# Performance work log

Measured on AMD Instinct MI355X. Metric: run time of the kernel, lower is better.

Reference implementation:

```python
import jax, jax.numpy as jnp
import numpy as np

B, N, F, T, K, O = 8, 1024, 64, 32, 3, 64


def setup_inputs() -> dict:
    key = jax.random.key(0)
    k0, k1, k2, k3 = jax.random.split(key, 4)
    x = jax.random.normal(k0, (B, N, F, T), dtype=jnp.float32)
    spatial_attention = jax.random.uniform(k1, (B, N, N), dtype=jnp.float32)
    cheb = jax.random.normal(k2, (K, N, N), dtype=jnp.float32) * 0.1  # stacked T_k
    Theta = jax.random.normal(k3, (K, F, O), dtype=jnp.float32) * (1.0 / np.sqrt(F))
    return {"x": x, "spatial_attention": spatial_attention, "cheb": cheb, "Theta": Theta}


def reference(x, spatial_attention, cheb, Theta):
    # Original per-timestep, per-k loop computes:
    #   rhs[b,i,f] = sum_j (T_k[j,i] * att[b,j,i])... note: T_k_with_at.permute(0,2,1) @ x
    #   i.e. rhs[b,i,f,t] = sum_j T_k[j,i]*att[b,j,i]*x[b,j,f,t]
    # Vectorized over all timesteps t and Chebyshev orders k at once.
    rhs = jnp.einsum('kji,bji,bjft->bkift', cheb, spatial_attention, x)  # (B,K,N,F,T)
    out = jnp.einsum('bkift,kfo->biot', rhs, Theta)                      # sum over k,f
    return jax.nn.relu(out)  # (B,N,O,T)
```

## Files before the change

kernel.cpp:

```cpp
#include <hip/hip_runtime.h>
#include <stdint.h>

#define Bn 8
#define Nn 1024
#define Fn 64
#define Tn 32
#define Kn 3
#define On 64
#define Rn (Kn * Nn)
#define Cn (On * Tn)
#define NT (Rn / 32)

typedef __bf16 bf16x8 __attribute__((ext_vector_type(8)));
typedef float f32x4 __attribute__((ext_vector_type(4)));
typedef __attribute__((address_space(1))) void gvoid;
typedef __attribute__((address_space(3))) void lvoid;

union BF8 { bf16x8 v; ushort s[8]; uint4 q; };

static __device__ __forceinline__ ushort f2bf(float f) {
  uint32_t u = __float_as_uint(f);
  return (ushort)((u + 0x7FFFu + ((u >> 16) & 1u)) >> 16);
}

static __device__ __forceinline__ void glds(const ushort* g, ushort* l) {
  __builtin_amdgcn_global_load_lds((gvoid*)g, (lvoid*)l, 16, 0, 0);
}

__global__ void k_thetaT(const float* __restrict__ Theta, ushort* __restrict__ ThT) {
  int idx = blockIdx.x * 256 + threadIdx.x;
  if (idx < Kn * On * Fn) {
    int k = idx / (On * Fn);
    int rem = idx % (On * Fn);
    int o = rem / Fn, f = rem % Fn;
    ThT[idx] = f2bf(Theta[(k * Fn + f) * On + o]);
  }
}

__global__ __launch_bounds__(256) void k_prepW(const float* __restrict__ att,
                                               const float* __restrict__ cheb,
                                               ushort* __restrict__ Wt) {
  __shared__ float tile[32][33];
  int i0 = blockIdx.x * 32, j0 = blockIdx.y * 32, b = blockIdx.z;
  int tid = threadIdx.x;
  int ci = tid & 31, rj = tid >> 5;
  float av[4];
#pragma unroll
  for (int p = 0; p < 4; p++) {
    int j = j0 + rj + p * 8;
    av[p] = att[((size_t)b * Nn + j) * Nn + i0 + ci];
  }
  for (int k = 0; k < Kn; k++) {
#pragma unroll
    for (int p = 0; p < 4; p++) {
      int j = j0 + rj + p * 8;
      tile[rj + p * 8][ci] = av[p] * cheb[((size_t)k * Nn + j) * Nn + i0 + ci];
    }
    __syncthreads();
#pragma unroll
    for (int p = 0; p < 4; p++) {
      int i = i0 + rj + p * 8;
      Wt[((size_t)b * Nn + i) * Rn + (size_t)k * Nn + j0 + ci] = f2bf(tile[ci][rj + p * 8]);
    }
    __syncthreads();
  }
}

__global__ __launch_bounds__(512) void k_prepY(const float* __restrict__ x,
                                               const ushort* __restrict__ ThT,
                                               ushort* __restrict__ Yt) {
  __shared__ ushort ylds[1024 * 32];
  int jt = blockIdx.x, b = blockIdx.y;
  int j0 = jt * 32;
  int tid = threadIdx.x;
  int lane = tid & 63, w = tid >> 6;
  int l15 = lane & 15, l4 = lane >> 4;

  BF8 bfr[4][2][2];
#pragma unroll
  for (int jj = 0; jj < 4; jj++) {
    const float* xp = x + ((size_t)b * Nn + (j0 + w * 4 + jj)) * (Fn * Tn);
#pragma unroll
    for (int ks = 0; ks < 2; ks++)
#pragma unroll
      for (int tf = 0; tf < 2; tf++) {
        int t = tf * 16 + l15;
        int fb = ks * 32 + l4 * 8;
#pragma unroll
        for (int e = 0; e < 8; e++)
          bfr[jj][ks][tf].s[e] = f2bf(xp[(fb + e) * Tn + t]);
      }
  }

  for (int k = 0; k < Kn; k++) {
    for (int h = 0; h < 2; h++) {
      BF8 afr[2][2];
#pragma unroll
      for (int o2 = 0; o2 < 2; o2++)
#pragma unroll
        for (int ks = 0; ks < 2; ks++) {
          int o = h * 32 + o2 * 16 + l15;
          afr[o2][ks].q = *(const uint4*)&ThT[((size_t)k * On + o) * Fn + ks * 32 + l4 * 8];
        }
#pragma unroll
      for (int jj = 0; jj < 4; jj++) {
        f32x4 acc[2][2] = {};
#pragma unroll
        for (int ks = 0; ks < 2; ks++)
#pragma unroll
          for (int o2 = 0; o2 < 2; o2++)
#pragma unroll
            for (int tf = 0; tf < 2; tf++)
              acc[o2][tf] = __builtin_amdgcn_mfma_f32_16x16x32_bf16(
                  afr[o2][ks].v, bfr[jj][ks][tf].v, acc[o2][tf], 0, 0, 0);
#pragma unroll
        for (int o2 = 0; o2 < 2; o2++)
#pragma unroll
          for (int tf = 0; tf < 2; tf++)
#pragma unroll
            for (int q = 0; q < 4; q++) {
              int cl = (o2 * 16 + l4 * 4 + q) * Tn + tf * 16 + l15;
              ylds[cl * 32 + w * 4 + jj] = f2bf(acc[o2][tf][q]);
            }
      }
      __syncthreads();
      const uint32_t* yl32 = (const uint32_t*)ylds;
      uint32_t* Yt32 = (uint32_t*)Yt;
      int e = tid & 15, rowst = tid >> 4;
      for (int pass = 0; pass < 32; pass++) {
        int cl = pass * 32 + rowst;
        size_t off = ((size_t)b * Cn + (size_t)(h * 1024 + cl)) * Rn + (size_t)k * Nn + j0;
        Yt32[off / 2 + e] = yl32[cl * 16 + e];
      }
      __syncthreads();
    }
  }
}

__global__ __launch_bounds__(512, 2) void k_gemm(const ushort* __restrict__ Wt,
                                                 const ushort* __restrict__ Yt,
                                                 float* __restrict__ out) {
  extern __shared__ __align__(16) ushort smem[];
  ushort* As = smem;
  ushort* Bs = smem + 32768;

  int g = blockIdx.x;
  int b = g & 7, slot = g >> 3;
  int i0 = (slot & 3) * 256, c0 = (slot >> 2) * 256;
  int tid = threadIdx.x, lane = tid & 63, w = tid >> 6;
  int l15 = lane & 15, l4 = lane >> 4;
  int wm = w >> 2, wn = w & 3;

  const ushort* Ab = Wt + ((size_t)b * Nn + i0) * Rn;
  const ushort* Bb = Yt + ((size_t)b * Cn + c0) * Rn;

  int srow = tid >> 2, sch = (tid & 3) * 8;
  const ushort* aS = Ab + (size_t)srow * Rn + sch;
  const ushort* bS = Bb + (size_t)srow * Rn + sch;
  int dst0 = w * 512;

  int abase = (wm * 128 + l15) * 32 + l4 * 8;
  int bbase = (wn * 64 + l15) * 32 + l4 * 8;

  f32x4 acc[8][4] = {};

#define STAGE_A(t) { int bo_ = ((t) & 3) * 8192; \
    glds(aS + (size_t)(t) * 32, As + bo_ + dst0); \
    glds(aS + 128 * (size_t)Rn + (size_t)(t) * 32, As + bo_ + 4096 + dst0); }
#define STAGE_B(t) { int bo_ = ((t) & 3) * 8192; \
    glds(bS + (size_t)(t) * 32, Bs + bo_ + dst0); \
    glds(bS + 128 * (size_t)Rn + (size_t)(t) * 32, Bs + bo_ + 4096 + dst0); }

  STAGE_A(0); STAGE_B(0);
  STAGE_A(1); STAGE_B(1);
  STAGE_A(2); STAGE_B(2);
  asm volatile("s_waitcnt vmcnt(8)" ::: "memory");
  __builtin_amdgcn_s_barrier();

#define WINDOW(t, DOSTAGE) { \
    int bo_ = ((t) & 3) * 8192; \
    const ushort* Abuf = As + bo_; \
    const ushort* Bbuf = Bs + bo_; \
    BF8 bf[4], af[8]; \
    _Pragma("unroll") for (int n = 0; n < 4; n++) \
      bf[n].q = *(const uint4*)&Bbuf[bbase + n * 512]; \
    _Pragma("unroll") for (int m = 0; m < 4; m++) \
      af[m].q = *(const uint4*)&Abuf[abase + m * 512]; \
    if (DOSTAGE) STAGE_A((t) + 3); \
    __builtin_amdgcn_s_setprio(1); \
    _Pragma("unroll") for (int m = 0; m < 4; m++) \
      _Pragma("unroll") for (int n = 0; n < 4; n++) \
        acc[m][n] = __builtin_amdgcn_mfma_f32_16x16x32_bf16(af[m].v, bf[n].v, acc[m][n], 0, 0, 0); \
    __builtin_amdgcn_s_setprio(0); \
    _Pragma("unroll") for (int m = 4; m < 8; m++) \
      af[m].q = *(const uint4*)&Abuf[abase + m * 512]; \
    if (DOSTAGE) STAGE_B((t) + 3); \
    __builtin_amdgcn_s_setprio(1); \
    _Pragma("unroll") for (int m = 4; m < 8; m++) \
      _Pragma("unroll") for (int n = 0; n < 4; n++) \
        acc[m][n] = __builtin_amdgcn_mfma_f32_16x16x32_bf16(af[m].v, bf[n].v, acc[m][n], 0, 0, 0); \
    __builtin_amdgcn_s_setprio(0); \
  }

  for (int t = 0; t < NT - 3; ++t) {
    WINDOW(t, 1);
    asm volatile("s_waitcnt vmcnt(8)" ::: "memory");
    __builtin_amdgcn_s_barrier();
  }
  WINDOW(NT - 3, 0);
  asm volatile("s_waitcnt vmcnt(4)" ::: "memory");
  __builtin_amdgcn_s_barrier();
  WINDOW(NT - 2, 0);
  asm volatile("s_waitcnt vmcnt(0)" ::: "memory");
  __builtin_amdgcn_s_barrier();
  WINDOW(NT - 1, 0);

#undef WINDOW
#undef STAGE_A
#undef STAGE_B

  float* ob = out + (size_t)b * Nn * Cn;
#pragma unroll
  for (int m = 0; m < 8; m++) {
    int i = i0 + wm * 128 + m * 16 + l4 * 4;
#pragma unroll
    for (int n = 0; n < 4; n++) {
      int c = c0 + wn * 64 + n * 16 + l15;
#pragma unroll
      for (int q = 0; q < 4; q++)
        ob[(size_t)(i + q) * Cn + c] = fmaxf(acc[m][n][q], 0.0f);
    }
  }
}

extern "C" void kernel_launch(void* const* d_in, const int* in_sizes, int n_in,
                              void* d_out, int out_size, void* d_ws, size_t ws_size,
                              hipStream_t stream) {
  const float* x     = (const float*)d_in[0];
  const float* att   = (const float*)d_in[1];
  const float* cheb  = (const float*)d_in[2];
  const float* Theta = (const float*)d_in[3];
  float* out = (float*)d_out;

  char* ws = (char*)d_ws;
  ushort* ThT = (ushort*)ws;
  ushort* Wt  = (ushort*)(ws + 65536);
  ushort* Yt  = (ushort*)(ws + 65536 + 50331648ull);

  hipFuncSetAttribute((const void*)k_gemm, hipFuncAttributeMaxDynamicSharedMemorySize, 131072);

  k_thetaT<<<48, 256, 0, stream>>>(Theta, ThT);
  k_prepW<<<dim3(32, 32, 8), 256, 0, stream>>>(att, cheb, Wt);
  k_prepY<<<dim3(32, 8), 512, 0, stream>>>(x, ThT, Yt);
  k_gemm<<<256, 512, 131072, stream>>>(Wt, Yt, out);
}
```

Baseline: 169.9 us.

## Restructure GEMM pipeline to K=64 double-buffered swizzled tiles and reuse cheb across batches

The main GEMM moves from 32-wide K steps with a 4-deep LDS ring to 64-wide K steps with double buffering and an XOR-swizzled LDS layout. Each tile is split into four quarter sub-phases that interleave LDS reads, async global-to-LDS staging and MFMA blocks, with barriers between phases. This aims to cut barrier count per FLOP and LDS bank conflicts. Separately, k_prepW loads the cheb values once and loops over batches, instead of re-reading cheb for every batch. In exchange there are more barriers per tile, and the hand-tuned vmcnt counts are fragile.

```diff
diff --git a/kernel.cpp b/kernel.cpp
--- a/kernel.cpp
+++ b/kernel.cpp
@@ -9,7 +9,7 @@
 #define On 64
 #define Rn (Kn * Nn)
 #define Cn (On * Tn)
-#define NT (Rn / 32)
+#define NT (Rn / 64)
 
 typedef __bf16 bf16x8 __attribute__((ext_vector_type(8)));
 typedef float f32x4 __attribute__((ext_vector_type(4)));
@@ -41,28 +41,36 @@
                                                const float* __restrict__ cheb,
                                                ushort* __restrict__ Wt) {
   __shared__ float tile[32][33];
-  int i0 = blockIdx.x * 32, j0 = blockIdx.y * 32, b = blockIdx.z;
+  int i0 = blockIdx.x * 32, j0 = blockIdx.y * 32;
   int tid = threadIdx.x;
   int ci = tid & 31, rj = tid >> 5;
-  float av[4];
+  float cv[4][Kn];
 #pragma unroll
   for (int p = 0; p < 4; p++) {
     int j = j0 + rj + p * 8;
-    av[p] = att[((size_t)b * Nn + j) * Nn + i0 + ci];
-  }
-  for (int k = 0; k < Kn; k++) {
+#pragma unroll
+    for (int k = 0; k < Kn; k++)
+      cv[p][k] = cheb[((size_t)k * Nn + j) * Nn + i0 + ci];
+  }
+  for (int b = 0; b < Bn; b++) {
+    float av[4];
 #pragma unroll
     for (int p = 0; p < 4; p++) {
       int j = j0 + rj + p * 8;
-      tile[rj + p * 8][ci] = av[p] * cheb[((size_t)k * Nn + j) * Nn + i0 + ci];
-    }
-    __syncthreads();
-#pragma unroll
-    for (int p = 0; p < 4; p++) {
-      int i = i0 + rj + p * 8;
-      Wt[((size_t)b * Nn + i) * Rn + (size_t)k * Nn + j0 + ci] = f2bf(tile[ci][rj + p * 8]);
-    }
-    __syncthreads();
+      av[p] = att[((size_t)b * Nn + j) * Nn + i0 + ci];
+    }
+    for (int k = 0; k < Kn; k++) {
+#pragma unroll
+      for (int p = 0; p < 4; p++)
+        tile[rj + p * 8][ci] = av[p] * cv[p][k];
+      __syncthreads();
+#pragma unroll
+      for (int p = 0; p < 4; p++) {
+        int i = i0 + rj + p * 8;
+        Wt[((size_t)b * Nn + i) * Rn + (size_t)k * Nn + j0 + ci] = f2bf(tile[ci][rj + p * 8]);
+      }
+      __syncthreads();
+    }
   }
 }
 
@@ -154,70 +162,90 @@
   const ushort* Ab = Wt + ((size_t)b * Nn + i0) * Rn;
   const ushort* Bb = Yt + ((size_t)b * Cn + c0) * Rn;
 
-  int srow = tid >> 2, sch = (tid & 3) * 8;
-  const ushort* aS = Ab + (size_t)srow * Rn + sch;
-  const ushort* bS = Bb + (size_t)srow * Rn + sch;
-  int dst0 = w * 512;
-
-  int abase = (wm * 128 + l15) * 32 + l4 * 8;
-  int bbase = (wn * 64 + l15) * 32 + l4 * 8;
+  int srcC = (((lane & 7) ^ (lane >> 3)) * 8);
+  int arow0 = w * 8 + (lane >> 3);
+  int brow0 = (w >> 2) * 64 + (w & 3) * 8 + (lane >> 3);
+
+  int aL = (wm * 64 + l15) * 64;
+  int bL = (wn * 32 + l15) * 64;
+  int x7 = l15 & 7;
+  int colx0 = ((l4) ^ x7) * 8;
+  int colx1 = ((4 + l4) ^ x7) * 8;
 
   f32x4 acc[8][4] = {};
-
-#define STAGE_A(t) { int bo_ = ((t) & 3) * 8192; \
-    glds(aS + (size_t)(t) * 32, As + bo_ + dst0); \
-    glds(aS + 128 * (size_t)Rn + (size_t)(t) * 32, As + bo_ + 4096 + dst0); }
-#define STAGE_B(t) { int bo_ = ((t) & 3) * 8192; \
-    glds(bS + (size_t)(t) * 32, Bs + bo_ + dst0); \
-    glds(bS + 128 * (size_t)Rn + (size_t)(t) * 32, Bs + bo_ + 4096 + dst0); }
-
-  STAGE_A(0); STAGE_B(0);
-  STAGE_A(1); STAGE_B(1);
-  STAGE_A(2); STAGE_B(2);
-  asm volatile("s_waitcnt vmcnt(8)" ::: "memory");
-  __builtin_amdgcn_s_barrier();
-
-#define WINDOW(t, DOSTAGE) { \
-    int bo_ = ((t) & 3) * 8192; \
-    const ushort* Abuf = As + bo_; \
-    const ushort* Bbuf = Bs + bo_; \
-    BF8 bf[4], af[8]; \
-    _Pragma("unroll") for (int n = 0; n < 4; n++) \
-      bf[n].q = *(const uint4*)&Bbuf[bbase + n * 512]; \
-    _Pragma("unroll") for (int m = 0; m < 4; m++) \
-      af[m].q = *(const uint4*)&Abuf[abase + m * 512]; \
-    if (DOSTAGE) STAGE_A((t) + 3); \
-    __builtin_amdgcn_s_setprio(1); \
-    _Pragma("unroll") for (int m = 0; m < 4; m++) \
-      _Pragma("unroll") for (int n = 0; n < 4; n++) \
-        acc[m][n] = __builtin_amdgcn_mfma_f32_16x16x32_bf16(af[m].v, bf[n].v, acc[m][n], 0, 0, 0); \
-    __builtin_amdgcn_s_setprio(0); \
-    _Pragma("unroll") for (int m = 4; m < 8; m++) \
-      af[m].q = *(const uint4*)&Abuf[abase + m * 512]; \
-    if (DOSTAGE) STAGE_B((t) + 3); \
-    __builtin_amdgcn_s_setprio(1); \
-    _Pragma("unroll") for (int m = 4; m < 8; m++) \
-      _Pragma("unroll") for (int n = 0; n < 4; n++) \
-        acc[m][n] = __builtin_amdgcn_mfma_f32_16x16x32_bf16(af[m].v, bf[n].v, acc[m][n], 0, 0, 0); \
-    __builtin_amdgcn_s_setprio(0); \
-  }
-
-  for (int t = 0; t < NT - 3; ++t) {
-    WINDOW(t, 1);
-    asm volatile("s_waitcnt vmcnt(8)" ::: "memory");
-    __builtin_amdgcn_s_barrier();
-  }
-  WINDOW(NT - 3, 0);
-  asm volatile("s_waitcnt vmcnt(4)" ::: "memory");
-  __builtin_amdgcn_s_barrier();
-  WINDOW(NT - 2, 0);
-  asm volatile("s_waitcnt vmcnt(0)" ::: "memory");
-  __builtin_amdgcn_s_barrier();
-  WINDOW(NT - 1, 0);
-
-#undef WINDOW
+  BF8 af[4][2], bf[4][2];
+
+#define MFMA_(a_, b_, c_) __builtin_amdgcn_mfma_f32_16x16x32_bf16((a_), (b_), (c_), 0, 0, 0)
+#define BAR() asm volatile("s_barrier" ::: "memory")
+#define PRIO1 __builtin_amdgcn_s_setprio(1)
+#define PRIO0 __builtin_amdgcn_s_setprio(0)
+
+#define STAGE_A(t_, h_) { int bo_ = ((t_) & 1) * 16384 + (h_) * 8192 + w * 512; \
+    const ushort* gp_ = Ab + (size_t)(arow0 + (h_) * 64) * Rn + (t_) * 64 + srcC; \
+    glds(gp_, As + bo_); \
+    glds(gp_ + 128 * (size_t)Rn, As + bo_ + 4096); }
+#define STAGE_B(t_, h_) { int bo_ = ((t_) & 1) * 16384 + (h_) * 8192 + w * 512; \
+    const ushort* gp_ = Bb + (size_t)(brow0 + (h_) * 32) * Rn + (t_) * 64 + srcC; \
+    glds(gp_, Bs + bo_); \
+    glds(gp_ + 128 * (size_t)Rn, Bs + bo_ + 4096); }
+
+#define RD_A(mh_) { _Pragma("unroll") for (int m = 0; m < 4; m++) { \
+    int ba_ = bufo + (mh_) * 8192 + aL + m * 1024; \
+    af[m][0].q = *(const uint4*)&As[ba_ + colx0]; \
+    af[m][1].q = *(const uint4*)&As[ba_ + colx1]; } }
+#define RD_B(nh_) { _Pragma("unroll") for (int n = 0; n < 2; n++) { \
+    int bb_ = bufo + (nh_) * 8192 + bL + n * 1024; \
+    bf[(nh_) * 2 + n][0].q = *(const uint4*)&Bs[bb_ + colx0]; \
+    bf[(nh_) * 2 + n][1].q = *(const uint4*)&Bs[bb_ + colx1]; } }
+#define MM(mh_, nh_) { _Pragma("unroll") for (int m = 0; m < 4; m++) \
+    _Pragma("unroll") for (int n = 0; n < 2; n++) { \
+      int gm_ = (mh_) * 4 + m, gn_ = (nh_) * 2 + n; \
+      acc[gm_][gn_] = MFMA_(af[m][0].v, bf[gn_][0].v, acc[gm_][gn_]); \
+      acc[gm_][gn_] = MFMA_(af[m][1].v, bf[gn_][1].v, acc[gm_][gn_]); } }
+
+#define VMC(n_) asm volatile("s_waitcnt vmcnt(" #n_ ")" ::: "memory")
+
+  STAGE_A(0, 0); STAGE_B(0, 0); STAGE_B(0, 1); STAGE_A(0, 1); STAGE_A(1, 0);
+  VMC(6);
+  BAR();
+
+#define TILE(t_, S1_, S2_, W0_, W1_, W3_, LAST_) { \
+    int bufo = ((t_) & 1) * 16384; \
+     \
+    RD_A(0); RD_B(0); \
+    if (S1_) STAGE_B((t_) + 1, 0); \
+    BAR(); \
+    PRIO1; MM(0, 0); PRIO0; \
+    VMC(W0_); BAR(); \
+     \
+    RD_B(1); \
+    if (S1_) { STAGE_B((t_) + 1, 1); STAGE_A((t_) + 1, 1); } \
+    BAR(); \
+    PRIO1; MM(0, 1); PRIO0; \
+    VMC(W1_); BAR(); \
+     \
+    RD_A(1); \
+    if (S2_) STAGE_A((t_) + 2, 0); \
+    BAR(); \
+    PRIO1; MM(1, 0); PRIO0; \
+    BAR(); \
+     \
+    PRIO1; MM(1, 1); PRIO0; \
+    if (!(LAST_)) { VMC(W3_); BAR(); } \
+  }
+
+  for (int t = 0; t < NT - 2; ++t)
+    TILE(t, 1, 1, 6, 8, 6, 0);
+  TILE(NT - 2, 1, 0, 6, 8, 4, 0);
+  TILE(NT - 1, 0, 0, 2, 0, 0, 1);
+
+#undef TILE
+#undef VMC
+#undef MM
+#undef RD_B
+#undef RD_A
+#undef STAGE_B
 #undef STAGE_A
-#undef STAGE_B
 
   float* ob = out + (size_t)b * Nn * Cn;
 #pragma unroll
@@ -250,7 +278,7 @@
   hipFuncSetAttribute((const void*)k_gemm, hipFuncAttributeMaxDynamicSharedMemorySize, 131072);
 
   k_thetaT<<<48, 256, 0, stream>>>(Theta, ThT);
-  k_prepW<<<dim3(32, 32, 8), 256, 0, stream>>>(att, cheb, Wt);
+  k_prepW<<<dim3(32, 32), 256, 0, stream>>>(att, cheb, Wt);
   k_prepY<<<dim3(32, 8), 512, 0, stream>>>(x, ThT, Yt);
   k_gemm<<<256, 512, 131072, stream>>>(Wt, Yt, out);
 }
```

New measurement: 175.5 us. +3.3%, slower.
